# Kernel optimization log

Measured on AMD Instinct MI355X. Metric: run time of the kernel, lower is better.

## Reference

```python
import jax, jax.numpy as jnp
import numpy as np
import math

B, S, D_MODEL, H = 128, 256, 128, 8
D_K = D_MODEL // H
FACTOR = 5
SAMPLE_K = FACTOR * int(math.ceil(math.log(S)))   # 30 sampled keys per query
N_TOP = min(FACTOR * int(math.ceil(math.log(S))), S)  # 30 active queries
KSIZE = 7


def setup_inputs() -> dict:
    key = jax.random.key(0)
    ks = jax.random.split(key, 10)
    s = 0.05
    return {
        "query": jax.random.normal(ks[0], (B, S, D_MODEL), jnp.float32),
        "key": jax.random.normal(ks[1], (B, S, D_MODEL), jnp.float32),
        "value": jax.random.normal(ks[2], (B, S, D_MODEL), jnp.float32),
        "conv_k_w": jax.random.normal(ks[3], (S, S, KSIZE), jnp.float32) * s,
        "conv_k_b": jax.random.normal(ks[4], (S,), jnp.float32) * s,
        "conv_v_w": jax.random.normal(ks[5], (S, S, KSIZE), jnp.float32) * s,
        "conv_v_b": jax.random.normal(ks[6], (S,), jnp.float32) * s,
        "lin_w": jax.random.normal(ks[7], (D_MODEL, D_MODEL), jnp.float32) * s,
        "lin_b": jax.random.normal(ks[8], (D_MODEL,), jnp.float32) * s,
        "index_sample": jax.random.randint(ks[9], (S, SAMPLE_K), 0, S),
    }


def _rotary(x):
    # x: [B,S,D]; complex rotation of consecutive pairs, angle = pos * theta^{-2i/D}
    half = D_MODEL // 2
    freqs = 1.0 / (10000.0 ** (jnp.arange(0, D_MODEL, 2, dtype=jnp.float32) / D_MODEL))
    ang = jnp.arange(S, dtype=jnp.float32)[:, None] * freqs[None, :]  # [S, half]
    cos, sin = jnp.cos(ang), jnp.sin(ang)
    xr = x.reshape(B, S, half, 2)
    out_r = xr[..., 0] * cos - xr[..., 1] * sin
    out_i = xr[..., 0] * sin + xr[..., 1] * cos
    return jnp.stack([out_r, out_i], axis=-1).reshape(B, S, D_MODEL)


def _causal_conv(x, w, b):
    # x: [B, C=S, L=D_MODEL]; causal => left-pad (KSIZE-1). w: [C_out, C_in, K]
    y = jax.lax.conv_general_dilated(
        x, w, window_strides=(1,), padding=[(KSIZE - 1, 0)],
        dimension_numbers=("NCH", "OIH", "NCH"))
    return y + b[None, :, None]


def reference(query, key, value, conv_k_w, conv_k_b, conv_v_w, conv_v_b,
              lin_w, lin_b, index_sample):
    q, k = _rotary(query), _rotary(key)
    k = _causal_conv(k, conv_k_w, conv_k_b)        # conv over seq-as-channels
    v = _causal_conv(value, conv_v_w, conv_v_b)
    # [B,S,D] -> [B,H,S,Dk]
    q = q.reshape(B, S, H, D_K).transpose(0, 2, 1, 3)
    k = k.reshape(B, S, H, D_K).transpose(0, 2, 1, 3)
    v = v.reshape(B, S, H, D_K).transpose(0, 2, 1, 3)

    # --- ProbSparse attention (Informer), mask=None ---
    k_sample = k[:, :, index_sample, :]                       # [B,H,S,SAMPLE_K,Dk]
    qk_sample = jnp.einsum('bhld,bhlsd->bhls', q, k_sample)   # sampled scores
    M = qk_sample.max(axis=-1) - qk_sample.mean(axis=-1)      # sparsity measure [B,H,S]
    _, m_top = jax.lax.top_k(M, N_TOP)                        # active queries [B,H,u]
    q_reduce = jnp.take_along_axis(q, m_top[..., None], axis=2)  # [B,H,u,Dk]
    scores = jnp.einsum('bhud,bhld->bhul', q_reduce, k) / jnp.sqrt(jnp.float32(D_K))
    attn = jax.nn.softmax(scores, axis=-1)
    out_top = jnp.einsum('bhul,bhld->bhud', attn, v)          # [B,H,u,Dk]
    # initial context = mean of V (no mask); overwrite rows of active queries
    context = jnp.broadcast_to(v.mean(axis=2, keepdims=True), (B, H, S, D_K))
    bi = jnp.arange(B)[:, None, None]
    hi = jnp.arange(H)[None, :, None]
    context = context.at[bi, hi, m_top].set(out_top)

    x = context.transpose(0, 2, 1, 3).reshape(B, S, D_MODEL)
    return x @ lin_w.T + lin_b
```

## Files before the change

### kernel.cpp

```cpp
#include <hip/hip_runtime.h>
#include <math.h>

constexpr int B_  = 128;
constexpr int S_  = 256;
constexpr int D_  = 128;
constexpr int H_  = 8;
constexpr int DK_ = 16;
constexpr int SK_ = 30;
constexpr int NT_ = 30;

typedef short short8  __attribute__((ext_vector_type(8)));
typedef float floatx4 __attribute__((ext_vector_type(4)));

__device__ inline ushort bf16_rne(float f) {
    unsigned u = __float_as_uint(f);
    u += 0x7fffu + ((u >> 16) & 1u);
    return (ushort)(u >> 16);
}
__device__ inline float bf16_to_f(ushort h) {
    return __uint_as_float(((unsigned)h) << 16);
}

__global__ __launch_bounds__(256) void wprep_kernel(
    const float* __restrict__ wk, const float* __restrict__ wv,
    const float* __restrict__ lw,
    ushort* __restrict__ wk_hi, ushort* __restrict__ wk_lo,
    ushort* __restrict__ wv_hi,
    ushort* __restrict__ lw_hi, ushort* __restrict__ lw_lo)
{
    int tid = blockIdx.x * 256 + threadIdx.x;
    if (tid < 131072) {
        int which = tid >> 16;
        int oi = tid & 65535;
        const float* src = (which ? wv : wk) + (size_t)oi * 7;
#pragma unroll
        for (int t = 0; t < 7; t++) {
            float f = src[t];
            ushort hi = bf16_rne(f);
            size_t dst = (size_t)t * 65536 + oi;
            if (which) {
                wv_hi[dst] = hi;
            } else {
                wk_hi[dst] = hi;
                wk_lo[dst] = bf16_rne(f - bf16_to_f(hi));
            }
        }
    } else {
        int ec = tid - 131072;
        float f = lw[ec];
        ushort hi = bf16_rne(f);
        lw_hi[ec] = hi;
        lw_lo[ec] = bf16_rne(f - bf16_to_f(hi));
    }
}

__global__ __launch_bounds__(256) void trig_kernel(float* __restrict__ tab)
{
    int tid = blockIdx.x * 256 + threadIdx.x;
    int f = tid & 63, l = tid >> 6;
    double freq = exp(((double)(-f) / 64.0) * 9.210340371976184);
    double ang  = (double)l * freq;
    tab[tid * 2]     = (float)cos(ang);
    tab[tid * 2 + 1] = (float)sin(ang);
}

__global__ __launch_bounds__(256) void rotary_kernel(
    const float* __restrict__ q, const float* __restrict__ k,
    const float* __restrict__ tab,
    float* __restrict__ q_h, float* __restrict__ k_rot)
{
    int tid = blockIdx.x * 256 + threadIdx.x;
    int f = tid & 63;
    int l = (tid >> 6) & 255;
    int b = tid >> 14;

    float2 cs = *(const float2*)(tab + (size_t)(l * 64 + f) * 2);
    float c = cs.x, s = cs.y;

    int base = (b * S_ + l) * D_ + 2 * f;
    float q0 = q[base], q1 = q[base + 1];
    float k0 = k[base], k1 = k[base + 1];

    float qr = q0 * c - q1 * s;
    float qi = q0 * s + q1 * c;
    float kr = k0 * c - k1 * s;
    float ki = k0 * s + k1 * c;

    k_rot[base]     = kr;
    k_rot[base + 1] = ki;

    int d = 2 * f;
    int h = d >> 4, dk = d & 15;
    int qb = ((b * H_ + h) * S_ + l) * DK_ + dk;
    q_h[qb]     = qr;
    q_h[qb + 1] = qi;
}

template<bool KP>
__global__ __launch_bounds__(256) void conv_mfma_kernel(
    const float* __restrict__ x, const ushort* __restrict__ whi,
    const ushort* __restrict__ wlo, const float* __restrict__ bias,
    float* __restrict__ yh)
{
    constexpr int LI = 72;
    __shared__ ushort xhi[134 * LI];
    __shared__ ushort xlo[KP ? 134 * LI : 8];

    int b    = blockIdx.x;
    int oblk = blockIdx.y * 64;
    int tid  = threadIdx.x;
    int lane = tid & 63, wid = tid >> 6;
    int lm = lane & 15, kb = lane >> 4;
    int ow = wid >> 1, dw = wid & 1;
    int obase = oblk + ow * 32;
    int dbase = dw * 64;

    floatx4 acc[8];
#pragma unroll
    for (int i = 0; i < 8; i++) acc[i] = (floatx4){0.f, 0.f, 0.f, 0.f};

    for (int idx = tid; idx < 6 * LI; idx += 256) {
        xhi[idx] = 0;
        if (KP) xlo[idx] = 0;
    }

    const ushort* abase_h = xhi + (dbase + lm) * LI + kb * 8;
    const ushort* abase_l = KP ? (xlo + (dbase + lm) * LI + kb * 8) : (const ushort*)0;

    for (int ic = 0; ic < 4; ic++) {
        __syncthreads();
        {
            int i = tid & 63, g = tid >> 6;
            const float4* src = (const float4*)(x + (((size_t)b * 256) + ic * 64 + i) * 128 + g * 32);
            ushort* dh = xhi + (g * 32 + 6) * LI + i;
            ushort* dl = KP ? (xlo + (g * 32 + 6) * LI + i) : (ushort*)0;
#pragma unroll
            for (int q8 = 0; q8 < 8; q8++) {
                float4 v4 = src[q8];
                float vv[4] = {v4.x, v4.y, v4.z, v4.w};
#pragma unroll
                for (int cc = 0; cc < 4; cc++) {
                    ushort hb = bf16_rne(vv[cc]);
                    dh[(q8 * 4 + cc) * LI] = hb;
                    if (KP) dl[(q8 * 4 + cc) * LI] = bf16_rne(vv[cc] - bf16_to_f(hb));
                }
            }
        }
        __syncthreads();
#pragma unroll
        for (int ks2 = 0; ks2 < 2; ks2++) {
            int ibase = ic * 64 + ks2 * 32 + kb * 8;
#pragma unroll
            for (int t = 0; t < 7; t++) {
                short8 xh[4], xl[4];
#pragma unroll
                for (int nd = 0; nd < 4; nd++) {
                    xh[nd] = *(const short8*)(abase_h + (nd * 16 + t) * LI + ks2 * 32);
                    if (KP) xl[nd] = *(const short8*)(abase_l + (nd * 16 + t) * LI + ks2 * 32);
                }
                short8 wh[2], wl[2];
#pragma unroll
                for (int po = 0; po < 2; po++) {
                    int o = obase + po * 16 + lm;
                    wh[po] = *(const short8*)(whi + (size_t)t * 65536 + o * 256 + ibase);
                    if (KP) wl[po] = *(const short8*)(wlo + (size_t)t * 65536 + o * 256 + ibase);
                }
#pragma unroll
                for (int po = 0; po < 2; po++) {
#pragma unroll
                    for (int nd = 0; nd < 4; nd++) {
                        int a = po * 4 + nd;
                        acc[a] = __builtin_amdgcn_mfma_f32_16x16x32_bf16(xh[nd], wh[po], acc[a], 0, 0, 0);
                        if (KP) {
                            acc[a] = __builtin_amdgcn_mfma_f32_16x16x32_bf16(xl[nd], wh[po], acc[a], 0, 0, 0);
                            acc[a] = __builtin_amdgcn_mfma_f32_16x16x32_bf16(xh[nd], wl[po], acc[a], 0, 0, 0);
                        }
                    }
                }
            }
        }
    }

#pragma unroll
    for (int po = 0; po < 2; po++) {
        int o = obase + po * 16 + lm;
        float bv = bias[o];
#pragma unroll
        for (int nd = 0; nd < 4; nd++) {
            int dhi = dw * 4 + nd;
#pragma unroll
            for (int r = 0; r < 4; r++) {
                int dk = kb * 4 + r;
                yh[(((size_t)b * 8 + dhi) * 256 + o) * 16 + dk] = acc[po * 4 + nd][r] + bv;
            }
        }
    }
}

__global__ __launch_bounds__(256) void topk_kernel(
    const float* __restrict__ q_h, const float* __restrict__ k_h,
    const int* __restrict__ idxs, int* __restrict__ sel)
{
    __shared__ float ks[S_ * 20];
    __shared__ float Marr[S_];
    __shared__ int cnt;
    int bh  = blockIdx.x;
    int tid = threadIdx.x;
    if (tid == 0) cnt = 0;

    const float* kp = k_h + (size_t)bh * S_ * DK_;
    for (int idx = tid; idx < S_ * DK_; idx += 256)
        ks[(idx >> 4) * 20 + (idx & 15)] = kp[idx];
    __syncthreads();

    float qr[16];
    const float4* qp = (const float4*)(q_h + ((size_t)bh * S_ + tid) * DK_);
#pragma unroll
    for (int i = 0; i < 4; i++) {
        float4 t4 = qp[i];
        qr[4*i] = t4.x; qr[4*i+1] = t4.y; qr[4*i+2] = t4.z; qr[4*i+3] = t4.w;
    }
    int idxr[SK_];
    const int* ip = idxs + tid * SK_;
#pragma unroll
    for (int s = 0; s < SK_; s++) idxr[s] = ip[s];

    float mx = -1e30f, sm = 0.f;
#pragma unroll
    for (int s = 0; s < SK_; s++) {
        const float4* kr = (const float4*)(ks + idxr[s] * 20);
        float4 k0 = kr[0], k1 = kr[1], k2 = kr[2], k3 = kr[3];
        float d0 = qr[0]*k0.x, d1 = qr[1]*k0.y, d2 = qr[2]*k0.z, d3 = qr[3]*k0.w;
        d0 = fmaf(qr[4],  k1.x, d0); d1 = fmaf(qr[5],  k1.y, d1);
        d2 = fmaf(qr[6],  k1.z, d2); d3 = fmaf(qr[7],  k1.w, d3);
        d0 = fmaf(qr[8],  k2.x, d0); d1 = fmaf(qr[9],  k2.y, d1);
        d2 = fmaf(qr[10], k2.z, d2); d3 = fmaf(qr[11], k2.w, d3);
        d0 = fmaf(qr[12], k3.x, d0); d1 = fmaf(qr[13], k3.y, d1);
        d2 = fmaf(qr[14], k3.z, d2); d3 = fmaf(qr[15], k3.w, d3);
        float dot = (d0 + d1) + (d2 + d3);
        mx = fmaxf(mx, dot);
        sm += dot;
    }
    float M = mx - sm * (1.0f / 30.0f);
    Marr[tid] = M;
    __syncthreads();

    int higher = 0;
    for (int j = 0; j < S_; j++) {
        float Mj = Marr[j];
        if (Mj > M || (Mj == M && j < tid)) higher++;
    }
    if (higher < NT_) {
        int slot = atomicAdd(&cnt, 1);
        sel[bh * NT_ + slot] = tid;
    }
}

__global__ __launch_bounds__(256) void attn_kernel(
    const float* __restrict__ q_h, const float* __restrict__ k_h,
    const float* __restrict__ v_h, const int* __restrict__ sel,
    ushort* __restrict__ ctx_hi, ushort* __restrict__ ctx_lo)
{
    __shared__ float ks[S_ * 20];
    __shared__ float vs[S_ * 20];
    __shared__ float P[NT_][S_ + 1];
    __shared__ float qs[NT_][16];
    __shared__ float partial[16][17];
    __shared__ float vmean_s[16];
    __shared__ int sel_s[NT_];
    __shared__ int selflag[S_];

    int bh = blockIdx.x, b = bh >> 3, h = bh & 7;
    int tid = threadIdx.x;

    const float* kp = k_h + (size_t)bh * S_ * DK_;
    const float* vp = v_h + (size_t)bh * S_ * DK_;
    for (int idx = tid; idx < S_ * DK_; idx += 256) {
        int r = idx >> 4, c = idx & 15;
        ks[r * 20 + c] = kp[idx];
        vs[r * 20 + c] = vp[idx];
    }
    selflag[tid] = 0;
    if (tid < NT_) sel_s[tid] = sel[bh * NT_ + tid];
    __syncthreads();
    if (tid < NT_) selflag[sel_s[tid]] = 1;
    for (int idx = tid; idx < NT_ * 16; idx += 256) {
        int u = idx >> 4, c = idx & 15;
        qs[u][c] = q_h[((size_t)bh * S_ + sel_s[u]) * DK_ + c];
    }
    {
        int dk = tid & 15, chunk = tid >> 4;
        float s = 0.f;
#pragma unroll
        for (int r = 0; r < 16; r++) s += vs[(chunk * 16 + r) * 20 + dk];
        partial[chunk][dk] = s;
    }
    __syncthreads();
    if (tid < 16) {
        float s = 0.f;
#pragma unroll
        for (int c = 0; c < 16; c++) s += partial[c][tid];
        vmean_s[tid] = s * (1.0f / 256.0f);
    }
    __syncthreads();

    if (!selflag[tid]) {
        alignas(16) ushort hh[16], ll[16];
#pragma unroll
        for (int i = 0; i < 16; i++) {
            float v = vmean_s[i];
            ushort hb = bf16_rne(v);
            hh[i] = hb;
            ll[i] = bf16_rne(v - bf16_to_f(hb));
        }
        size_t off = ((size_t)(b * S_ + tid)) * D_ + h * DK_;
        ((uint4*)(ctx_hi + off))[0] = ((uint4*)hh)[0];
        ((uint4*)(ctx_hi + off))[1] = ((uint4*)hh)[1];
        ((uint4*)(ctx_lo + off))[0] = ((uint4*)ll)[0];
        ((uint4*)(ctx_lo + off))[1] = ((uint4*)ll)[1];
    }

    int g = tid >> 3, j = tid & 7;
    if (g < NT_) {
        float qreg[16];
        const float4* q4 = (const float4*)qs[g];
#pragma unroll
        for (int i = 0; i < 4; i++) {
            float4 t4 = q4[i];
            qreg[4*i] = t4.x; qreg[4*i+1] = t4.y; qreg[4*i+2] = t4.z; qreg[4*i+3] = t4.w;
        }
        float sc[32];
        float mx = -1e30f;
#pragma unroll
        for (int li = 0; li < 32; li++) {
            int l = j + li * 8;
            const float4* kr = (const float4*)(ks + l * 20);
            float4 k0 = kr[0], k1 = kr[1], k2 = kr[2], k3 = kr[3];
            float d0 = qreg[0]*k0.x, d1 = qreg[1]*k0.y, d2 = qreg[2]*k0.z, d3 = qreg[3]*k0.w;
            d0 = fmaf(qreg[4],  k1.x, d0); d1 = fmaf(qreg[5],  k1.y, d1);
            d2 = fmaf(qreg[6],  k1.z, d2); d3 = fmaf(qreg[7],  k1.w, d3);
            d0 = fmaf(qreg[8],  k2.x, d0); d1 = fmaf(qreg[9],  k2.y, d1);
            d2 = fmaf(qreg[10], k2.z, d2); d3 = fmaf(qreg[11], k2.w, d3);
            d0 = fmaf(qreg[12], k3.x, d0); d1 = fmaf(qreg[13], k3.y, d1);
            d2 = fmaf(qreg[14], k3.z, d2); d3 = fmaf(qreg[15], k3.w, d3);
            sc[li] = ((d0 + d1) + (d2 + d3)) * 0.25f;
            mx = fmaxf(mx, sc[li]);
        }
        mx = fmaxf(mx, __shfl_xor(mx, 1));
        mx = fmaxf(mx, __shfl_xor(mx, 2));
        mx = fmaxf(mx, __shfl_xor(mx, 4));
        float se = 0.f;
#pragma unroll
        for (int li = 0; li < 32; li++) {
            float e = __expf(sc[li] - mx);
            P[g][j + li * 8] = e;
            se += e;
        }
        se += __shfl_xor(se, 1);
        se += __shfl_xor(se, 2);
        se += __shfl_xor(se, 4);
        float inv = 1.0f / se;

        int dk0 = j * 2;
        float o0 = 0.f, o1 = 0.f;
#pragma unroll 8
        for (int l = 0; l < S_; l++) {
            float p = P[g][l];
            float2 vv = *(const float2*)(vs + l * 20 + dk0);
            o0 = fmaf(p, vv.x, o0);
            o1 = fmaf(p, vv.y, o1);
        }
        int lrow = sel_s[g];
        float v0 = o0 * inv, v1 = o1 * inv;
        ushort h0 = bf16_rne(v0), h1 = bf16_rne(v1);
        ushort l0 = bf16_rne(v0 - bf16_to_f(h0));
        ushort l1 = bf16_rne(v1 - bf16_to_f(h1));
        size_t off = ((size_t)(b * S_ + lrow)) * D_ + h * DK_ + dk0;
        *(uint*)(ctx_hi + off) = (uint)h0 | ((uint)h1 << 16);
        *(uint*)(ctx_lo + off) = (uint)l0 | ((uint)l1 << 16);
    }
}

__global__ __launch_bounds__(256) void linear_mfma_kernel(
    const ushort* __restrict__ ctx_hi, const ushort* __restrict__ ctx_lo,
    const ushort* __restrict__ w_hi, const ushort* __restrict__ w_lo,
    const float* __restrict__ bias, float* __restrict__ out)
{
    __shared__ ushort ahi[128 * 136];
    __shared__ ushort alo[128 * 136];

    int tid  = threadIdx.x;
    int lane = tid & 63, wid = tid >> 6;
    int lm = lane & 15, kb = lane >> 4;
    size_t rowbase = (size_t)blockIdx.x * 128;

    for (int idx = tid; idx < 2048; idx += 256) {
        int row = idx >> 4, c16 = idx & 15;
        short8 vh = *(const short8*)(ctx_hi + (rowbase + row) * 128 + c16 * 8);
        short8 vl = *(const short8*)(ctx_lo + (rowbase + row) * 128 + c16 * 8);
        *(short8*)(ahi + row * 136 + c16 * 8) = vh;
        *(short8*)(alo + row * 136 + c16 * 8) = vl;
    }
    __syncthreads();

    floatx4 acc[16];
#pragma unroll
    for (int i = 0; i < 16; i++) acc[i] = (floatx4){0.f, 0.f, 0.f, 0.f};

    const ushort* arow_h = ahi + (wid * 32 + lm) * 136 + kb * 8;
    const ushort* arow_l = alo + (wid * 32 + lm) * 136 + kb * 8;

#pragma unroll
    for (int kstep = 0; kstep < 4; kstep++) {
        short8 afh[2], afl[2];
#pragma unroll
        for (int mf = 0; mf < 2; mf++) {
            afh[mf] = *(const short8*)(arow_h + mf * 16 * 136 + kstep * 32);
            afl[mf] = *(const short8*)(arow_l + mf * 16 * 136 + kstep * 32);
        }
        short8 bfh[8], bfl[8];
#pragma unroll
        for (int nf = 0; nf < 8; nf++) {
            const ushort* wp = w_hi + (size_t)(nf * 16 + lm) * 128 + kstep * 32 + kb * 8;
            const ushort* wq = w_lo + (size_t)(nf * 16 + lm) * 128 + kstep * 32 + kb * 8;
            bfh[nf] = *(const short8*)wp;
            bfl[nf] = *(const short8*)wq;
        }
#pragma unroll
        for (int mf = 0; mf < 2; mf++) {
#pragma unroll
            for (int nf = 0; nf < 8; nf++) {
                int a = mf * 8 + nf;
                acc[a] = __builtin_amdgcn_mfma_f32_16x16x32_bf16(afh[mf], bfh[nf], acc[a], 0, 0, 0);
                acc[a] = __builtin_amdgcn_mfma_f32_16x16x32_bf16(afl[mf], bfh[nf], acc[a], 0, 0, 0);
                acc[a] = __builtin_amdgcn_mfma_f32_16x16x32_bf16(afh[mf], bfl[nf], acc[a], 0, 0, 0);
            }
        }
    }

#pragma unroll
    for (int nf = 0; nf < 8; nf++) {
        int col = nf * 16 + lm;
        float bv = bias[col];
#pragma unroll
        for (int mf = 0; mf < 2; mf++) {
#pragma unroll
            for (int r = 0; r < 4; r++) {
                int row = wid * 32 + mf * 16 + kb * 4 + r;
                out[(rowbase + row) * 128 + col] = acc[mf * 8 + nf][r] + bv;
            }
        }
    }
}

extern "C" void kernel_launch(void* const* d_in, const int* in_sizes, int n_in,
                              void* d_out, int out_size, void* d_ws, size_t ws_size,
                              hipStream_t stream)
{
    const float* query = (const float*)d_in[0];
    const float* key   = (const float*)d_in[1];
    const float* value = (const float*)d_in[2];
    const float* ckw   = (const float*)d_in[3];
    const float* ckb   = (const float*)d_in[4];
    const float* cvw   = (const float*)d_in[5];
    const float* cvb   = (const float*)d_in[6];
    const float* lw    = (const float*)d_in[7];
    const float* lb    = (const float*)d_in[8];
    const int*   isamp = (const int*)d_in[9];
    float* out = (float*)d_out;
    float* ws  = (float*)d_ws;

    const size_t NBSD = (size_t)B_ * S_ * D_;
    float* q_h  = ws;
    float* kbuf = ws + NBSD;
    float* k_h  = ws + 2 * NBSD;
    float* v_h  = ws + 3 * NBSD;
    int*   sel  = (int*)(ws + 4 * NBSD);
    ushort* wk_hi = (ushort*)(sel + B_ * H_ * NT_);
    ushort* wk_lo = wk_hi + 7 * 65536;
    ushort* wv_hi = wk_lo + 7 * 65536;
    ushort* lw_hi = wv_hi + 7 * 65536;
    ushort* lw_lo = lw_hi + 16384;
    float*  trig  = (float*)(lw_lo + 16384);
    ushort* ctx_hi = (ushort*)kbuf;
    ushort* ctx_lo = ctx_hi + NBSD;

    wprep_kernel<<<dim3(576), 256, 0, stream>>>(ckw, cvw, lw, wk_hi, wk_lo, wv_hi, lw_hi, lw_lo);
    trig_kernel<<<dim3(64), 256, 0, stream>>>(trig);
    rotary_kernel<<<dim3((B_ * S_ * 64) / 256), 256, 0, stream>>>(query, key, trig, q_h, kbuf);
    conv_mfma_kernel<true ><<<dim3(B_, 4), 256, 0, stream>>>(kbuf,  wk_hi, wk_lo, ckb, k_h);
    conv_mfma_kernel<false><<<dim3(B_, 4), 256, 0, stream>>>(value, wv_hi, wv_hi, cvb, v_h);
    topk_kernel<<<dim3(B_ * H_), 256, 0, stream>>>(q_h, k_h, isamp, sel);
    attn_kernel<<<dim3(B_ * H_), 256, 0, stream>>>(q_h, k_h, v_h, sel, ctx_hi, ctx_lo);
    linear_mfma_kernel<<<dim3(256), 256, 0, stream>>>(ctx_hi, ctx_lo, lw_hi, lw_lo, lb, out);
}
```

Baseline: 285.3 us.

## Pre-transpose and bf16-split conv inputs, retile causal conv over D dimension

```diff
diff --git a/kernel.cpp b/kernel.cpp
--- a/kernel.cpp
+++ b/kernel.cpp
@@ -96,103 +96,122 @@
     q_h[qb + 1] = qi;
 }
 
+__global__ __launch_bounds__(256) void transcvt_kernel(
+    const float* __restrict__ k_rot, const float* __restrict__ value,
+    ushort* __restrict__ khi_t, ushort* __restrict__ klo_t,
+    ushort* __restrict__ vhi_t)
+{
+    __shared__ float tile[64 * 132];
+    int b = blockIdx.x;
+    int which = blockIdx.y;
+    int tid = threadIdx.x;
+    const float* src = which ? value : k_rot;
+
+    for (int lc = 0; lc < 4; lc++) {
+        __syncthreads();
+        for (int s = tid; s < 2048; s += 256) {
+            int l = s >> 5, c4 = s & 31;
+            *(float4*)(tile + l * 132 + c4 * 4) =
+                *(const float4*)(src + (((size_t)b * 256) + lc * 64 + l) * 128 + c4 * 4);
+        }
+        __syncthreads();
+        int d = tid >> 1, half = tid & 1;
+        alignas(16) ushort hh[32], ll[32];
+#pragma unroll
+        for (int j = 0; j < 32; j++) {
+            float f = tile[(half * 32 + j) * 132 + d];
+            ushort hb = bf16_rne(f);
+            hh[j] = hb;
+            ll[j] = bf16_rne(f - bf16_to_f(hb));
+        }
+        size_t off = (((size_t)b * 128) + d) * 256 + lc * 64 + half * 32;
+        if (which) {
+#pragma unroll
+            for (int m = 0; m < 4; m++) ((uint4*)(vhi_t + off))[m] = ((uint4*)hh)[m];
+        } else {
+#pragma unroll
+            for (int m = 0; m < 4; m++) ((uint4*)(khi_t + off))[m] = ((uint4*)hh)[m];
+#pragma unroll
+            for (int m = 0; m < 4; m++) ((uint4*)(klo_t + off))[m] = ((uint4*)ll)[m];
+        }
+    }
+}
+
 template<bool KP>
-__global__ __launch_bounds__(256) void conv_mfma_kernel(
-    const float* __restrict__ x, const ushort* __restrict__ whi,
-    const ushort* __restrict__ wlo, const float* __restrict__ bias,
-    float* __restrict__ yh)
+__global__ __launch_bounds__(256, 4) void conv2_kernel(
+    const ushort* __restrict__ xhi_g, const ushort* __restrict__ xlo_g,
+    const ushort* __restrict__ whi, const ushort* __restrict__ wlo,
+    const float* __restrict__ bias, float* __restrict__ yh)
 {
     constexpr int LI = 72;
-    __shared__ ushort xhi[134 * LI];
-    __shared__ ushort xlo[KP ? 134 * LI : 8];
-
-    int b    = blockIdx.x;
-    int oblk = blockIdx.y * 64;
-    int tid  = threadIdx.x;
+    __shared__ ushort xhi[70 * LI];
+    __shared__ ushort xlo[KP ? 70 * LI : 8];
+
+    int b   = blockIdx.x;
+    int ob  = blockIdx.y * 64;
+    int db  = blockIdx.z * 64;
+    int tid = threadIdx.x;
     int lane = tid & 63, wid = tid >> 6;
     int lm = lane & 15, kb = lane >> 4;
-    int ow = wid >> 1, dw = wid & 1;
-    int obase = oblk + ow * 32;
-    int dbase = dw * 64;
-
-    floatx4 acc[8];
-#pragma unroll
-    for (int i = 0; i < 8; i++) acc[i] = (floatx4){0.f, 0.f, 0.f, 0.f};
-
-    for (int idx = tid; idx < 6 * LI; idx += 256) {
-        xhi[idx] = 0;
-        if (KP) xlo[idx] = 0;
-    }
-
-    const ushort* abase_h = xhi + (dbase + lm) * LI + kb * 8;
-    const ushort* abase_l = KP ? (xlo + (dbase + lm) * LI + kb * 8) : (const ushort*)0;
+
+    floatx4 acc[4];
+#pragma unroll
+    for (int i = 0; i < 4; i++) acc[i] = (floatx4){0.f, 0.f, 0.f, 0.f};
+
+    const short8 zero8 = {0, 0, 0, 0, 0, 0, 0, 0};
 
     for (int ic = 0; ic < 4; ic++) {
         __syncthreads();
-        {
-            int i = tid & 63, g = tid >> 6;
-            const float4* src = (const float4*)(x + (((size_t)b * 256) + ic * 64 + i) * 128 + g * 32);
-            ushort* dh = xhi + (g * 32 + 6) * LI + i;
-            ushort* dl = KP ? (xlo + (g * 32 + 6) * LI + i) : (ushort*)0;
-#pragma unroll
-            for (int q8 = 0; q8 < 8; q8++) {
-                float4 v4 = src[q8];
-                float vv[4] = {v4.x, v4.y, v4.z, v4.w};
-#pragma unroll
-                for (int cc = 0; cc < 4; cc++) {
-                    ushort hb = bf16_rne(vv[cc]);
-                    dh[(q8 * 4 + cc) * LI] = hb;
-                    if (KP) dl[(q8 * 4 + cc) * LI] = bf16_rne(vv[cc] - bf16_to_f(hb));
+        for (int s = tid; s < 560; s += 256) {
+            int r = s >> 3, p = s & 7;
+            int col = db - 6 + r;
+            size_t goff = (((size_t)b * 128) + col) * 256 + ic * 64 + p * 8;
+            short8 vh = (col >= 0) ? *(const short8*)(xhi_g + goff) : zero8;
+            *(short8*)(xhi + r * LI + p * 8) = vh;
+            if (KP) {
+                short8 vl = (col >= 0) ? *(const short8*)(xlo_g + goff) : zero8;
+                *(short8*)(xlo + r * LI + p * 8) = vl;
+            }
+        }
+        __syncthreads();
+#pragma unroll
+        for (int ks2 = 0; ks2 < 2; ks2++) {
+#pragma unroll
+            for (int t = 0; t < 7; t++) {
+                int arow = (wid * 16 + lm + t) * LI + ks2 * 32 + kb * 8;
+                short8 ah = *(const short8*)(xhi + arow);
+                short8 al;
+                if (KP) al = *(const short8*)(xlo + arow);
+
+                short8 bh[4], bl[4];
+#pragma unroll
+                for (int nf = 0; nf < 4; nf++) {
+                    size_t woff = (size_t)t * 65536 + (size_t)(ob + nf * 16 + lm) * 256
+                                + ic * 64 + ks2 * 32 + kb * 8;
+                    bh[nf] = *(const short8*)(whi + woff);
+                    if (KP) bl[nf] = *(const short8*)(wlo + woff);
                 }
-            }
-        }
-        __syncthreads();
-#pragma unroll
-        for (int ks2 = 0; ks2 < 2; ks2++) {
-            int ibase = ic * 64 + ks2 * 32 + kb * 8;
-#pragma unroll
-            for (int t = 0; t < 7; t++) {
-                short8 xh[4], xl[4];
-#pragma unroll
-                for (int nd = 0; nd < 4; nd++) {
-                    xh[nd] = *(const short8*)(abase_h + (nd * 16 + t) * LI + ks2 * 32);
-                    if (KP) xl[nd] = *(const short8*)(abase_l + (nd * 16 + t) * LI + ks2 * 32);
-                }
-                short8 wh[2], wl[2];
-#pragma unroll
-                for (int po = 0; po < 2; po++) {
-                    int o = obase + po * 16 + lm;
-                    wh[po] = *(const short8*)(whi + (size_t)t * 65536 + o * 256 + ibase);
-                    if (KP) wl[po] = *(const short8*)(wlo + (size_t)t * 65536 + o * 256 + ibase);
-                }
-#pragma unroll
-                for (int po = 0; po < 2; po++) {
-#pragma unroll
-                    for (int nd = 0; nd < 4; nd++) {
-                        int a = po * 4 + nd;
-                        acc[a] = __builtin_amdgcn_mfma_f32_16x16x32_bf16(xh[nd], wh[po], acc[a], 0, 0, 0);
-                        if (KP) {
-                            acc[a] = __builtin_amdgcn_mfma_f32_16x16x32_bf16(xl[nd], wh[po], acc[a], 0, 0, 0);
-                            acc[a] = __builtin_amdgcn_mfma_f32_16x16x32_bf16(xh[nd], wl[po], acc[a], 0, 0, 0);
-                        }
+#pragma unroll
+                for (int nf = 0; nf < 4; nf++) {
+                    acc[nf] = __builtin_amdgcn_mfma_f32_16x16x32_bf16(ah, bh[nf], acc[nf], 0, 0, 0);
+                    if (KP) {
+                        acc[nf] = __builtin_amdgcn_mfma_f32_16x16x32_bf16(al, bh[nf], acc[nf], 0, 0, 0);
+                        acc[nf] = __builtin_amdgcn_mfma_f32_16x16x32_bf16(ah, bl[nf], acc[nf], 0, 0, 0);
                     }
                 }
             }
         }
     }
 
-#pragma unroll
-    for (int po = 0; po < 2; po++) {
-        int o = obase + po * 16 + lm;
+    int hidx = (db >> 4) + wid;
+#pragma unroll
+    for (int nf = 0; nf < 4; nf++) {
+        int o = ob + nf * 16 + lm;
         float bv = bias[o];
 #pragma unroll
-        for (int nd = 0; nd < 4; nd++) {
-            int dhi = dw * 4 + nd;
-#pragma unroll
-            for (int r = 0; r < 4; r++) {
-                int dk = kb * 4 + r;
-                yh[(((size_t)b * 8 + dhi) * 256 + o) * 16 + dk] = acc[po * 4 + nd][r] + bv;
-            }
+        for (int r = 0; r < 4; r++) {
+            int dk = kb * 4 + r;
+            yh[(((size_t)b * 8 + hidx) * 256 + o) * 16 + dk] = acc[nf][r] + bv;
         }
     }
 }
@@ -421,10 +440,8 @@
         short8 bfh[8], bfl[8];
 #pragma unroll
         for (int nf = 0; nf < 8; nf++) {
-            const ushort* wp = w_hi + (size_t)(nf * 16 + lm) * 128 + kstep * 32 + kb * 8;
-            const ushort* wq = w_lo + (size_t)(nf * 16 + lm) * 128 + kstep * 32 + kb * 8;
-            bfh[nf] = *(const short8*)wp;
-            bfl[nf] = *(const short8*)wq;
+            bfh[nf] = *(const short8*)(w_hi + (size_t)(nf * 16 + lm) * 128 + kstep * 32 + kb * 8);
+            bfl[nf] = *(const short8*)(w_lo + (size_t)(nf * 16 + lm) * 128 + kstep * 32 + kb * 8);
         }
 #pragma unroll
         for (int mf = 0; mf < 2; mf++) {
@@ -482,14 +499,18 @@
     ushort* lw_hi = wv_hi + 7 * 65536;
     ushort* lw_lo = lw_hi + 16384;
     float*  trig  = (float*)(lw_lo + 16384);
+    ushort* khi_t = (ushort*)(trig + 32768);
+    ushort* klo_t = khi_t + NBSD;
+    ushort* vhi_t = klo_t + NBSD;
     ushort* ctx_hi = (ushort*)kbuf;
     ushort* ctx_lo = ctx_hi + NBSD;
 
     wprep_kernel<<<dim3(576), 256, 0, stream>>>(ckw, cvw, lw, wk_hi, wk_lo, wv_hi, lw_hi, lw_lo);
     trig_kernel<<<dim3(64), 256, 0, stream>>>(trig);
     rotary_kernel<<<dim3((B_ * S_ * 64) / 256), 256, 0, stream>>>(query, key, trig, q_h, kbuf);
-    conv_mfma_kernel<true ><<<dim3(B_, 4), 256, 0, stream>>>(kbuf,  wk_hi, wk_lo, ckb, k_h);
-    conv_mfma_kernel<false><<<dim3(B_, 4), 256, 0, stream>>>(value, wv_hi, wv_hi, cvb, v_h);
+    transcvt_kernel<<<dim3(B_, 2), 256, 0, stream>>>(kbuf, value, khi_t, klo_t, vhi_t);
+    conv2_kernel<true ><<<dim3(B_, 4, 2), 256, 0, stream>>>(khi_t, klo_t, wk_hi, wk_lo, ckb, k_h);
+    conv2_kernel<false><<<dim3(B_, 4, 2), 256, 0, stream>>>(vhi_t, vhi_t, wv_hi, wv_hi, cvb, v_h);
     topk_kernel<<<dim3(B_ * H_), 256, 0, stream>>>(q_h, k_h, isamp, sel);
     attn_kernel<<<dim3(B_ * H_), 256, 0, stream>>>(q_h, k_h, v_h, sel, ctx_hi, ctx_lo);
     linear_mfma_kernel<<<dim3(256), 256, 0, stream>>>(ctx_hi, ctx_lo, lw_hi, lw_lo, lb, out);
```

After: 530.5 us. 85.9% more time.

## Pre-transpose conv inputs to bf16 and merge K/V convs into one launch

Applied to the files above, without the earlier changes.

```diff
diff --git a/kernel.cpp b/kernel.cpp
--- a/kernel.cpp
+++ b/kernel.cpp
@@ -96,15 +96,64 @@
     q_h[qb + 1] = qi;
 }
 
-template<bool KP>
-__global__ __launch_bounds__(256) void conv_mfma_kernel(
-    const float* __restrict__ x, const ushort* __restrict__ whi,
-    const ushort* __restrict__ wlo, const float* __restrict__ bias,
-    float* __restrict__ yh)
+__global__ __launch_bounds__(256) void transcvt_kernel(
+    const float* __restrict__ k_rot, const float* __restrict__ value,
+    ushort* __restrict__ khi_t, ushort* __restrict__ klo_t,
+    ushort* __restrict__ vhi_t)
+{
+    __shared__ float tile[64 * 132];
+    int b = blockIdx.x;
+    int which = blockIdx.y;
+    int tid = threadIdx.x;
+    const float* src = which ? value : k_rot;
+
+    for (int lc = 0; lc < 4; lc++) {
+        __syncthreads();
+        for (int s = tid; s < 2048; s += 256) {
+            int l = s >> 5, c4 = s & 31;
+            *(float4*)(tile + l * 132 + c4 * 4) =
+                *(const float4*)(src + (((size_t)b * 256) + lc * 64 + l) * 128 + c4 * 4);
+        }
+        __syncthreads();
+        int d = tid >> 1, half = tid & 1;
+        alignas(16) ushort hh[32], ll[32];
+#pragma unroll
+        for (int j = 0; j < 32; j++) {
+            float f = tile[(half * 32 + j) * 132 + d];
+            ushort hb = bf16_rne(f);
+            hh[j] = hb;
+            ll[j] = bf16_rne(f - bf16_to_f(hb));
+        }
+        size_t off = (((size_t)b * 128) + d) * 256 + lc * 64 + half * 32;
+        if (which) {
+#pragma unroll
+            for (int m = 0; m < 4; m++) ((uint4*)(vhi_t + off))[m] = ((uint4*)hh)[m];
+        } else {
+#pragma unroll
+            for (int m = 0; m < 4; m++) ((uint4*)(khi_t + off))[m] = ((uint4*)hh)[m];
+#pragma unroll
+            for (int m = 0; m < 4; m++) ((uint4*)(klo_t + off))[m] = ((uint4*)ll)[m];
+        }
+    }
+}
+
+__global__ __launch_bounds__(256, 4) void conv3_kernel(
+    const ushort* __restrict__ khi_t, const ushort* __restrict__ klo_t,
+    const ushort* __restrict__ vhi_t,
+    const ushort* __restrict__ wk_hi, const ushort* __restrict__ wk_lo,
+    const ushort* __restrict__ wv_hi,
+    const float* __restrict__ kbias, const float* __restrict__ vbias,
+    float* __restrict__ k_h, float* __restrict__ v_h)
 {
     constexpr int LI = 72;
     __shared__ ushort xhi[134 * LI];
-    __shared__ ushort xlo[KP ? 134 * LI : 8];
+    __shared__ ushort xlo[134 * LI];
+
+    const bool kp = (blockIdx.z == 0);
+    const ushort* xhi_g = kp ? khi_t : vhi_t;
+    const ushort* whi   = kp ? wk_hi : wv_hi;
+    const float*  bias  = kp ? kbias : vbias;
+    float* yh           = kp ? k_h : v_h;
 
     int b    = blockIdx.x;
     int oblk = blockIdx.y * 64;
@@ -119,32 +168,19 @@
 #pragma unroll
     for (int i = 0; i < 8; i++) acc[i] = (floatx4){0.f, 0.f, 0.f, 0.f};
 
-    for (int idx = tid; idx < 6 * LI; idx += 256) {
-        xhi[idx] = 0;
-        if (KP) xlo[idx] = 0;
-    }
+    for (int idx = tid; idx < 6 * LI; idx += 256) { xhi[idx] = 0; xlo[idx] = 0; }
 
     const ushort* abase_h = xhi + (dbase + lm) * LI + kb * 8;
-    const ushort* abase_l = KP ? (xlo + (dbase + lm) * LI + kb * 8) : (const ushort*)0;
+    const ushort* abase_l = xlo + (dbase + lm) * LI + kb * 8;
 
     for (int ic = 0; ic < 4; ic++) {
         __syncthreads();
-        {
-            int i = tid & 63, g = tid >> 6;
-            const float4* src = (const float4*)(x + (((size_t)b * 256) + ic * 64 + i) * 128 + g * 32);
-            ushort* dh = xhi + (g * 32 + 6) * LI + i;
-            ushort* dl = KP ? (xlo + (g * 32 + 6) * LI + i) : (ushort*)0;
-#pragma unroll
-            for (int q8 = 0; q8 < 8; q8++) {
-                float4 v4 = src[q8];
-                float vv[4] = {v4.x, v4.y, v4.z, v4.w};
-#pragma unroll
-                for (int cc = 0; cc < 4; cc++) {
-                    ushort hb = bf16_rne(vv[cc]);
-                    dh[(q8 * 4 + cc) * LI] = hb;
-                    if (KP) dl[(q8 * 4 + cc) * LI] = bf16_rne(vv[cc] - bf16_to_f(hb));
-                }
-            }
+        for (int s = tid; s < 1024; s += 256) {
+            int d = s >> 3, p = s & 7;
+            size_t g = (((size_t)b * 128) + d) * 256 + ic * 64 + p * 8;
+            *(short8*)(xhi + (d + 6) * LI + p * 8) = *(const short8*)(xhi_g + g);
+            if (kp)
+                *(short8*)(xlo + (d + 6) * LI + p * 8) = *(const short8*)(klo_t + g);
         }
         __syncthreads();
 #pragma unroll
@@ -156,14 +192,14 @@
 #pragma unroll
                 for (int nd = 0; nd < 4; nd++) {
                     xh[nd] = *(const short8*)(abase_h + (nd * 16 + t) * LI + ks2 * 32);
-                    if (KP) xl[nd] = *(const short8*)(abase_l + (nd * 16 + t) * LI + ks2 * 32);
+                    if (kp) xl[nd] = *(const short8*)(abase_l + (nd * 16 + t) * LI + ks2 * 32);
                 }
                 short8 wh[2], wl[2];
 #pragma unroll
                 for (int po = 0; po < 2; po++) {
-                    int o = obase + po * 16 + lm;
-                    wh[po] = *(const short8*)(whi + (size_t)t * 65536 + o * 256 + ibase);
-                    if (KP) wl[po] = *(const short8*)(wlo + (size_t)t * 65536 + o * 256 + ibase);
+                    size_t woff = (size_t)t * 65536 + (size_t)(obase + po * 16 + lm) * 256 + ibase;
+                    wh[po] = *(const short8*)(whi + woff);
+                    if (kp) wl[po] = *(const short8*)(wk_lo + woff);
                 }
 #pragma unroll
                 for (int po = 0; po < 2; po++) {
@@ -171,7 +207,7 @@
                     for (int nd = 0; nd < 4; nd++) {
                         int a = po * 4 + nd;
                         acc[a] = __builtin_amdgcn_mfma_f32_16x16x32_bf16(xh[nd], wh[po], acc[a], 0, 0, 0);
-                        if (KP) {
+                        if (kp) {
                             acc[a] = __builtin_amdgcn_mfma_f32_16x16x32_bf16(xl[nd], wh[po], acc[a], 0, 0, 0);
                             acc[a] = __builtin_amdgcn_mfma_f32_16x16x32_bf16(xh[nd], wl[po], acc[a], 0, 0, 0);
                         }
@@ -421,10 +457,8 @@
         short8 bfh[8], bfl[8];
 #pragma unroll
         for (int nf = 0; nf < 8; nf++) {
-            const ushort* wp = w_hi + (size_t)(nf * 16 + lm) * 128 + kstep * 32 + kb * 8;
-            const ushort* wq = w_lo + (size_t)(nf * 16 + lm) * 128 + kstep * 32 + kb * 8;
-            bfh[nf] = *(const short8*)wp;
-            bfl[nf] = *(const short8*)wq;
+            bfh[nf] = *(const short8*)(w_hi + (size_t)(nf * 16 + lm) * 128 + kstep * 32 + kb * 8);
+            bfl[nf] = *(const short8*)(w_lo + (size_t)(nf * 16 + lm) * 128 + kstep * 32 + kb * 8);
         }
 #pragma unroll
         for (int mf = 0; mf < 2; mf++) {
@@ -482,14 +516,19 @@
     ushort* lw_hi = wv_hi + 7 * 65536;
     ushort* lw_lo = lw_hi + 16384;
     float*  trig  = (float*)(lw_lo + 16384);
+    ushort* khi_t = (ushort*)(trig + 32768);
+    ushort* klo_t = khi_t + NBSD;
+    ushort* vhi_t = klo_t + NBSD;
     ushort* ctx_hi = (ushort*)kbuf;
     ushort* ctx_lo = ctx_hi + NBSD;
 
     wprep_kernel<<<dim3(576), 256, 0, stream>>>(ckw, cvw, lw, wk_hi, wk_lo, wv_hi, lw_hi, lw_lo);
     trig_kernel<<<dim3(64), 256, 0, stream>>>(trig);
     rotary_kernel<<<dim3((B_ * S_ * 64) / 256), 256, 0, stream>>>(query, key, trig, q_h, kbuf);
-    conv_mfma_kernel<true ><<<dim3(B_, 4), 256, 0, stream>>>(kbuf,  wk_hi, wk_lo, ckb, k_h);
-    conv_mfma_kernel<false><<<dim3(B_, 4), 256, 0, stream>>>(value, wv_hi, wv_hi, cvb, v_h);
+    transcvt_kernel<<<dim3(B_, 2), 256, 0, stream>>>(kbuf, value, khi_t, klo_t, vhi_t);
+    conv3_kernel<<<dim3(B_, 4, 2), 256, 0, stream>>>(khi_t, klo_t, vhi_t,
+                                                     wk_hi, wk_lo, wv_hi,
+                                                     ckb, cvb, k_h, v_h);
     topk_kernel<<<dim3(B_ * H_), 256, 0, stream>>>(q_h, k_h, isamp, sel);
     attn_kernel<<<dim3(B_ * H_), 256, 0, stream>>>(q_h, k_h, v_h, sel, ctx_hi, ctx_lo);
     linear_mfma_kernel<<<dim3(256), 256, 0, stream>>>(ctx_hi, ctx_lo, lw_hi, lw_lo, lb, out);
```

Result: no change. 284.5 us (-0.3%).
